# Optimization experiments

Measured on AMD Instinct MI355X. Metric: run time of the kernel, lower is better.

Reference implementation:

```python
import jax, jax.numpy as jnp
import numpy as np

B, C, N, T = 32, 32, 300, 64      # batch, residual/conv channels, nodes, seq_len
DIM, K, SKIP, GD = 40, 20, 64, 2  # node_dim, top-k (subgraph_size), skip_channels, gcn_depth
TANH_A, PROP_A = 3.0, 0.05
KSET = (2, 3, 6, 7)
TOUT = T - (KSET[-1] - 1)          # 58: time length after dilated inception (dilation=1)


def conv2d(x, w, b):
    y = jax.lax.conv_general_dilated(x, w, (1, 1), 'VALID', dimension_numbers=('NCHW', 'OIHW', 'NCHW'))
    return y + b[None, :, None, None]


def setup_inputs() -> dict:
    key = jax.random.key(0)
    ks = iter(jax.random.split(key, 48))
    def nrm(shape, s=1.0):
        return jax.random.normal(next(ks), shape, jnp.float32) * s
    inp = {
        'x': nrm((B, C, N, T)),
        'x_skip': nrm((B, SKIP, N, 1)),
        'idx': jnp.arange(N, dtype=jnp.int32),
        'emb1': nrm((N, DIM), 0.1), 'emb2': nrm((N, DIM), 0.1),
        'lin1_w': nrm((DIM, DIM), 0.15), 'lin1_b': jnp.zeros((DIM,), jnp.float32),
        'lin2_w': nrm((DIM, DIM), 0.15), 'lin2_b': jnp.zeros((DIM,), jnp.float32),
        'skip_w': nrm((SKIP, C, 1, TOUT), 0.05), 'skip_b': jnp.zeros((SKIP,), jnp.float32),
        'mp1_w': nrm((C, (GD + 1) * C, 1, 1), 0.1), 'mp1_b': jnp.zeros((C,), jnp.float32),
        'mp2_w': nrm((C, (GD + 1) * C, 1, 1), 0.1), 'mp2_b': jnp.zeros((C,), jnp.float32),
        'ln_w': jnp.ones((C, N, TOUT), jnp.float32), 'ln_b': jnp.zeros((C, N, TOUT), jnp.float32),
    }
    for k in KSET:
        inp[f'fw{k}'] = nrm((C // 4, C, 1, k), 0.1); inp[f'fb{k}'] = jnp.zeros((C // 4,), jnp.float32)
        inp[f'gw{k}'] = nrm((C // 4, C, 1, k), 0.1); inp[f'gb{k}'] = jnp.zeros((C // 4,), jnp.float32)
    return inp


def _forward(x, x_skip, idx, emb1, emb2, lin1_w, lin1_b, lin2_w, lin2_b,
             fws, gws, skip_w, skip_b, mp1_w, mp1_b, mp2_w, mp2_b, ln_w, ln_b):
    # --- GraphConstructor: learned sparse adjacency via tanh/relu/top-k/scatter ---
    n1 = jnp.tanh(TANH_A * (emb1[idx] @ lin1_w.T + lin1_b))
    n2 = jnp.tanh(TANH_A * (emb2[idx] @ lin2_w.T + lin2_b))
    a = n1 @ n2.T - n2 @ n1.T
    A = jax.nn.relu(jnp.tanh(TANH_A * a))
    _, cols = jax.lax.top_k(A, K)                               # [N, K] per-row top-k indices
    mask = jnp.zeros_like(A).at[jnp.arange(N)[:, None], cols].set(1.0)
    A = A * mask
    # --- DilatedInception filter/gate (Conv2d kernel (1,k), crop to shortest) ---
    Xf = jnp.tanh(jnp.concatenate([conv2d(x, w, b)[..., -TOUT:] for w, b in fws], axis=1))
    Xg = jax.nn.sigmoid(jnp.concatenate([conv2d(x, w, b)[..., -TOUT:] for w, b in gws], axis=1))
    X = Xf * Xg                                                 # dropout is identity (training=False)
    X_skip_out = conv2d(X, skip_w, skip_b) + x_skip             # [B, SKIP, N, 1]
    # --- MixProp graph diffusion over A and A^T ---
    def mixprop(Xin, Adj, w, b):
        Ah = Adj + jnp.eye(N, dtype=Adj.dtype)
        Ah = Ah / Ah.sum(1)[:, None]                            # row-normalize
        H, hops = Xin, [Xin]
        for _ in range(GD):
            H = PROP_A * Xin + (1.0 - PROP_A) * jnp.einsum('bcwt,vw->bcvt', H, Ah)
            hops.append(H)
        return conv2d(jnp.concatenate(hops, axis=1), w, b)      # 1x1 conv: (GD+1)*C -> C
    X = mixprop(X, A, mp1_w, mp1_b) + mixprop(X, A.T, mp2_w, mp2_b)
    X = X + x[..., -TOUT:]
    # --- LayerNorm over (C, N, TOUT) with node-indexed affine ---
    mu = X.mean(axis=(1, 2, 3), keepdims=True)
    var = ((X - mu) ** 2).mean(axis=(1, 2, 3), keepdims=True)
    Xn = (X - mu) * jax.lax.rsqrt(var + 1e-5)
    X = Xn * ln_w[:, idx, :][None] + ln_b[:, idx, :][None]
    return X, X_skip_out


def reference(x, x_skip, idx, emb1, emb2, lin1_w, lin1_b, lin2_w, lin2_b,
              fw2, fb2, fw3, fb3, fw6, fb6, fw7, fb7,
              gw2, gb2, gw3, gb3, gw6, gb6, gw7, gb7,
              skip_w, skip_b, mp1_w, mp1_b, mp2_w, mp2_b, ln_w, ln_b):
    fws = [(fw2, fb2), (fw3, fb3), (fw6, fb6), (fw7, fb7)]
    gws = [(gw2, gb2), (gw3, gb3), (gw6, gb6), (gw7, gb7)]
    return _forward(x, x_skip, idx, emb1, emb2, lin1_w, lin1_b, lin2_w, lin2_b,
                    fws, gws, skip_w, skip_b, mp1_w, mp1_b, mp2_w, mp2_b, ln_w, ln_b)
```

## Files before the change

### kernel.cpp

```cpp
#include <hip/hip_runtime.h>
#include <hip/hip_bf16.h>
#include <math.h>

typedef __hip_bfloat16 bf16;
typedef __attribute__((ext_vector_type(8))) short bf16x8;
typedef __attribute__((ext_vector_type(4))) float f32x4;

#define NB 32
#define NC 32
#define NNODE 300
#define NT 64
#define NDIM 40
#define KTOP 20
#define NSKIP 64
#define NTOUT 58
#define SLAB 17400
#define BSLAB 556800
#define XEL 17817600
#define PSLAB 2048
#define BPSLAB 614400
#define XPEL 19660800

__device__ __forceinline__ float b2f(bf16 v){ return __bfloat162float(v); }
__device__ __forceinline__ bf16 f2b(float v){ return __float2bfloat16(v); }
__device__ __forceinline__ float fsig(float x){ return 1.0f/(1.0f + __expf(-x)); }
__device__ __forceinline__ float ftanh(float x){ return 2.0f*fsig(2.0f*x) - 1.0f; }

__device__ __forceinline__ unsigned short bbits(float v){
  bf16 h = f2b(v); unsigned short s; __builtin_memcpy(&s, &h, 2); return s;
}

__device__ __forceinline__ void fma8(float acc[8], uint4 d, float vv){
  acc[0] = fmaf(vv, __uint_as_float(d.x << 16),          acc[0]);
  acc[1] = fmaf(vv, __uint_as_float(d.x & 0xffff0000u),  acc[1]);
  acc[2] = fmaf(vv, __uint_as_float(d.y << 16),          acc[2]);
  acc[3] = fmaf(vv, __uint_as_float(d.y & 0xffff0000u),  acc[3]);
  acc[4] = fmaf(vv, __uint_as_float(d.z << 16),          acc[4]);
  acc[5] = fmaf(vv, __uint_as_float(d.z & 0xffff0000u),  acc[5]);
  acc[6] = fmaf(vv, __uint_as_float(d.w << 16),          acc[6]);
  acc[7] = fmaf(vv, __uint_as_float(d.w & 0xffff0000u),  acc[7]);
}

__device__ __forceinline__ void unp8(float f[8], uint4 d){
  f[0] = __uint_as_float(d.x << 16); f[1] = __uint_as_float(d.x & 0xffff0000u);
  f[2] = __uint_as_float(d.y << 16); f[3] = __uint_as_float(d.y & 0xffff0000u);
  f[4] = __uint_as_float(d.z << 16); f[5] = __uint_as_float(d.z & 0xffff0000u);
  f[6] = __uint_as_float(d.w << 16); f[7] = __uint_as_float(d.w & 0xffff0000u);
}

__device__ __forceinline__ uint4 pack8(const float f[8]){
  uint4 d;
  d.x = (unsigned)bbits(f[0]) | ((unsigned)bbits(f[1]) << 16);
  d.y = (unsigned)bbits(f[2]) | ((unsigned)bbits(f[3]) << 16);
  d.z = (unsigned)bbits(f[4]) | ((unsigned)bbits(f[5]) << 16);
  d.w = (unsigned)bbits(f[6]) | ((unsigned)bbits(f[7]) << 16);
  return d;
}

__device__ __forceinline__ void bv_swz(int bid, int& b, int& v){
  int xcd = bid & 7, i = bid >> 3;
  int nb = xcd*1200 + i;
  b = nb / NNODE; v = nb - b*NNODE;
}

__global__ void k_nodes(const float* __restrict__ emb1, const float* __restrict__ emb2,
                        const float* __restrict__ l1w, const float* __restrict__ l1b,
                        const float* __restrict__ l2w, const float* __restrict__ l2b,
                        const int* __restrict__ idxp,
                        float* __restrict__ n1, float* __restrict__ n2){
  int i = blockIdx.x; int d = threadIdx.x;
  if (d >= NDIM) return;
  int r = idxp[i];
  float a1 = l1b[d], a2 = l2b[d];
  for (int k=0;k<NDIM;++k){
    a1 = fmaf(emb1[r*NDIM+k], l1w[d*NDIM+k], a1);
    a2 = fmaf(emb2[r*NDIM+k], l2w[d*NDIM+k], a2);
  }
  n1[i*NDIM+d] = tanhf(3.0f*a1);
  n2[i*NDIM+d] = tanhf(3.0f*a2);
}

__global__ void __launch_bounds__(64) k_adjrow(const float* __restrict__ n1,
                                               const float* __restrict__ n2,
                                               float* __restrict__ Am){
  int i = blockIdx.x; int lane = threadIdx.x;
  __shared__ float rowo[NNODE];
  __shared__ float rowv[NNODE];
  __shared__ int   sel[NNODE];
  for (int j=lane;j<NNODE;j+=64){
    float a = 0.f;
    #pragma unroll
    for (int k=0;k<NDIM;++k){
      float a1 = n1[i*NDIM+k], a2 = n2[i*NDIM+k];
      a = fmaf(a1, n2[j*NDIM+k], a);
      a = fmaf(-a2, n1[j*NDIM+k], a);
    }
    float v = tanhf(3.0f*a);
    v = v > 0.f ? v : 0.f;
    rowo[j]=v; rowv[j]=v; sel[j]=0;
  }
  __syncthreads();
  for (int it=0; it<KTOP; ++it){
    float best = -1.f; int bi = 0x7fffffff;
    for (int j=lane;j<NNODE;j+=64){
      float v = rowv[j];
      if (v > best){ best=v; bi=j; }
    }
    #pragma unroll
    for (int off=32; off; off>>=1){
      float ov = __shfl_xor(best, off);
      int   oi = __shfl_xor(bi, off);
      if (ov > best || (ov == best && oi < bi)){ best=ov; bi=oi; }
    }
    if (lane==0){ sel[bi]=1; rowv[bi]=-2.f; }
    __syncthreads();
  }
  for (int j=lane;j<NNODE;j+=64)
    Am[i*NNODE+j] = sel[j] ? rowo[j] : 0.f;
}

__global__ void __launch_bounds__(64) k_csr(const float* __restrict__ Am,
                                            int* __restrict__ aidx, float* __restrict__ aval,
                                            int* __restrict__ acnt){
  int r = blockIdx.x; int lane = threadIdx.x;
  int v = (r < NNODE) ? r : r - NNODE;
  int*   ip = aidx + r*304;
  float* vp = aval + r*304;
  if (lane==0){ ip[0]=v; vp[0]=1.0f; }
  int cnt = 1; float s = 1.0f;
  for (int base=0; base<NNODE; base+=64){
    int j = base + lane; float val = 0.f; bool p = false;
    if (j < NNODE){
      val = (r < NNODE) ? Am[v*NNODE + j] : Am[j*NNODE + v];
      p = val > 0.f;
    }
    unsigned long long m = __ballot(p);
    int pre = __popcll(m & ((1ull << lane) - 1ull));
    if (p){ ip[cnt+pre]=j; vp[cnt+pre]=val; }
    cnt += __popcll(m);
    float vs = p ? val : 0.f;
    #pragma unroll
    for (int off=32; off; off>>=1) vs += __shfl_xor(vs, off);
    s += vs;
  }
  for (int e=lane; e<cnt; e+=64) vp[e] = vp[e] / s;
  if (lane==0) acnt[r]=cnt;
}

__global__ void k_wpack2(const float* __restrict__ fw2,const float* __restrict__ fw3,
                         const float* __restrict__ fw6,const float* __restrict__ fw7,
                         const float* __restrict__ gw2,const float* __restrict__ gw3,
                         const float* __restrict__ gw6,const float* __restrict__ gw7,
                         const float* __restrict__ fb2,const float* __restrict__ fb3,
                         const float* __restrict__ fb6,const float* __restrict__ fb7,
                         const float* __restrict__ gb2,const float* __restrict__ gb3,
                         const float* __restrict__ gb6,const float* __restrict__ gb7,
                         bf16* __restrict__ wfA, float* __restrict__ biasPk){
  int T = blockIdx.x*blockDim.x + threadIdx.x;
  if (T < 14336){
    int j = T & 7;
    int q = T >> 3;
    int l = q & 63; q >>= 6;
    int ks = q % 7, mt = q / 7;
    int m = mt*16 + (l & 15);
    int k = ks*32 + (l >> 4)*8 + j;
    int c = m >> 1, path = m & 1;
    int cls = c >> 3, o = c & 7;
    int ic = k / 7, d = k - ic*7;
    int kk = (cls==0) ? 2 : (cls==1) ? 3 : (cls==2) ? 6 : 7;
    int tp = d - (7 - kk);
    float val = 0.f;
    if (tp >= 0){
      const float* w = (path==0)
        ? (cls==0?fw2:cls==1?fw3:cls==2?fw6:fw7)
        : (cls==0?gw2:cls==1?gw3:cls==2?gw6:gw7);
      val = w[(o*NC + ic)*kk + tp];
    }
    wfA[T] = f2b(val);
  } else if (T < 14336 + 32){
    int c = T - 14336;
    int cls = c >> 3, o = c & 7;
    const float* fb = cls==0?fb2:cls==1?fb3:cls==2?fb6:fb7;
    const float* gb = cls==0?gb2:cls==1?gb3:cls==2?gb6:gb7;
    biasPk[c*2]   = fb[o];
    biasPk[c*2+1] = gb[o];
  }
}

__global__ void k_wprepM(const float* __restrict__ m1w, const float* __restrict__ m2w,
                         const float* __restrict__ m1b, const float* __restrict__ m2b,
                         bf16* __restrict__ pkB, float* __restrict__ biasSum){
  int id = blockIdx.x*blockDim.x + threadIdx.x;
  if (id < 5120){
    int j = id & 7, l = (id >> 3) & 63, q = id >> 9;
    int ks = q % 5, nt = q / 5;
    int k = (l >> 4)*8 + j;
    int c = nt*16 + (l & 15);
    float val;
    if      (ks == 0) val = m1w[c*96 + k] + m2w[c*96 + k];
    else if (ks == 1) val = m1w[c*96 + 32 + k];
    else if (ks == 2) val = m1w[c*96 + 64 + k];
    else if (ks == 3) val = m2w[c*96 + 32 + k];
    else              val = m2w[c*96 + 64 + k];
    pkB[id] = f2b(val);
  } else if (id < 5152){
    int c = id - 5120;
    biasSum[c] = m1b[c] + m2b[c];
  }
}

__global__ void k_wTb(const float* __restrict__ sw, bf16* __restrict__ wTb){
  int id = blockIdx.x*blockDim.x + threadIdx.x;
  if (id >= 131072) return;
  int j = id & 7, l = (id >> 3) & 63, q = id >> 9;
  int ks = q & 63, nt = q >> 6;
  int k = ks*32 + (l >> 4)*8 + j;
  int t = k >> 5, c = k & 31;
  int sc = nt*16 + (l & 15);
  float val = (t < NTOUT) ? sw[sc*1856 + c*NTOUT + t] : 0.f;
  wTb[id] = f2b(val);
}

__global__ void __launch_bounds__(256) k_incepM(const float* __restrict__ x,
    const bf16* __restrict__ wfA, const float* __restrict__ biasPk,
    bf16* __restrict__ Xp){
  __shared__ bf16 xsb[32*72];
  __shared__ uint4 xim2[28*64];
  int b, n; bv_swz(blockIdx.x, b, n);
  int bn = b*NNODE + n;
  int tid = threadIdx.x;
  {
    int c = tid >> 3, t0 = (tid & 7)*8;
    const float* src = x + ((size_t)(b*NC + c)*NNODE + n)*NT + t0;
    float4 v0 = *reinterpret_cast<const float4*>(src);
    float4 v1 = *reinterpret_cast<const float4*>(src + 4);
    float f[8] = {v0.x,v0.y,v0.z,v0.w,v1.x,v1.y,v1.z,v1.w};
    *reinterpret_cast<uint4*>(&xsb[c*72 + t0]) = pack8(f);
    if ((tid & 7) == 7)
      *reinterpret_cast<uint4*>(&xsb[c*72 + 64]) = make_uint4(0,0,0,0);
  }
  __syncthreads();
  #pragma unroll
  for (int i=0;i<7;++i){
    int pr = tid + i*256;
    int kb = pr >> 6, t = pr & 63;
    int k0 = kb*8;
    int ic = k0 / 7, d = k0 - ic*7;
    unsigned sh[8];
    #pragma unroll
    for (int j=0;j<8;++j){
      sh[j] = *reinterpret_cast<const unsigned short*>(&xsb[ic*72 + t + d]);
      ++d; if (d == 7){ d = 0; ++ic; }
    }
    xim2[kb*64 + t] = make_uint4(sh[0]|(sh[1]<<16), sh[2]|(sh[3]<<16),
                                 sh[4]|(sh[5]<<16), sh[6]|(sh[7]<<16));
  }
  __syncthreads();
  int lane = tid & 63;
  int mt = __builtin_amdgcn_readfirstlane(tid >> 6);
  bf16x8 wA[7];
  #pragma unroll
  for (int ks=0; ks<7; ++ks)
    wA[ks] = *reinterpret_cast<const bf16x8*>(wfA + (size_t)((mt*7 + ks)*64 + lane)*8);
  int g = lane >> 4;
  int c0 = mt*8 + 2*g;
  float4 bias2 = *reinterpret_cast<const float4*>(biasPk + c0*2);
  #pragma unroll
  for (int nt=0; nt<4; ++nt){
    int t = (lane & 15) + nt*16;
    f32x4 acc = {0.f, 0.f, 0.f, 0.f};
    #pragma unroll
    for (int ks=0; ks<7; ++ks){
      bf16x8 bfr = __builtin_bit_cast(bf16x8, xim2[(ks*4 + g)*64 + t]);
      acc = __builtin_amdgcn_mfma_f32_16x16x32_bf16(wA[ks], bfr, acc, 0, 0, 0);
    }
    bool act = t < NTOUT;
    float X0 = act ? (ftanh(acc[0] + bias2.x) * fsig(acc[1] + bias2.y)) : 0.f;
    float X1 = act ? (ftanh(acc[2] + bias2.z) * fsig(acc[3] + bias2.w)) : 0.f;
    unsigned pv = (unsigned)bbits(X0) | ((unsigned)bbits(X1) << 16);
    *reinterpret_cast<unsigned*>(Xp + (size_t)bn*PSLAB + t*32 + c0) = pv;
  }
}

__global__ void __launch_bounds__(256) k_skipM(const bf16* __restrict__ Xp, const bf16* __restrict__ wTb,
      const float* __restrict__ skip_b, const float* __restrict__ x_skip, float* __restrict__ out){
  int bn0 = blockIdx.x * 16;
  int tid = threadIdx.x, lane = tid & 63;
  int nt = __builtin_amdgcn_readfirstlane(tid >> 6);
  int g = lane >> 4, col = lane & 15;
  const bf16* aptr = Xp + (size_t)(bn0 + col)*PSLAB + g*8;
  const bf16* bptr = wTb + ((size_t)nt*64*64 + lane)*8;
  f32x4 acc = {0.f, 0.f, 0.f, 0.f};
  #pragma unroll 4
  for (int ks=0; ks<64; ++ks){
    bf16x8 aF = *reinterpret_cast<const bf16x8*>(aptr + ks*32);
    bf16x8 bF = *reinterpret_cast<const bf16x8*>(bptr + (size_t)ks*512);
    acc = __builtin_amdgcn_mfma_f32_16x16x32_bf16(aF, bF, acc, 0, 0, 0);
  }
  int sc = nt*16 + col;
  float sb = skip_b[sc];
  #pragma unroll
  for (int r=0;r<4;++r){
    int bn = bn0 + g*4 + r;
    int b = bn / NNODE, n = bn - b*NNODE;
    size_t so = (size_t)b*NSKIP*NNODE + (size_t)sc*NNODE + n;
    out[(size_t)XEL + so] = acc[r] + sb + x_skip[so];
  }
}

__global__ void __launch_bounds__(256) k_prop(const bf16* __restrict__ Xp,
    bf16* __restrict__ HA0, bf16* __restrict__ HA1,
    const int* __restrict__ aidx, const float* __restrict__ aval, const int* __restrict__ acnt){
  __shared__ int   sidx[304];
  __shared__ float sval[304];
  int bid = blockIdx.x;
  int xcd = bid & 7, i = bid >> 3;
  int side = i & 1, jj = i >> 1;
  int nb = xcd*1200 + jj;
  int b = nb / NNODE, v = nb - b*NNODE;
  int r = (side ? NNODE : 0) + v;
  bf16* HA = side ? HA1 : HA0;
  int cnt = acnt[r];
  for (int e = threadIdx.x; e < cnt; e += 256){
    sidx[e] = aidx[r*304 + e] * PSLAB;
    sval[e] = aval[r*304 + e];
  }
  __syncthreads();
  int t = threadIdx.x >> 2, cb = threadIdx.x & 3;
  int off = t*32 + cb*8;
  const bf16* base = Xp + (size_t)b*BPSLAB + off;
  float acc[8] = {0,0,0,0,0,0,0,0};
  #pragma unroll 4
  for (int j=0;j<cnt;++j){
    uint4 d = *reinterpret_cast<const uint4*>(base + sidx[j]);
    fma8(acc, d, sval[j]);
  }
  size_t own = (size_t)b*BPSLAB + (size_t)v*PSLAB + off;
  uint4 dx = *reinterpret_cast<const uint4*>(Xp + own);
  float xf[8]; unp8(xf, dx);
  float h[8];
  #pragma unroll
  for (int k=0;k<8;++k) h[k] = fmaf(0.95f, acc[k], 0.05f*xf[k]);
  *reinterpret_cast<uint4*>(HA + own) = pack8(h);
}

__global__ void __launch_bounds__(256) k_fuse(const bf16* __restrict__ Xp,
    const bf16* __restrict__ HA0, const bf16* __restrict__ HA1,
    float* __restrict__ out, const float* __restrict__ x,
    const int* __restrict__ aidx, const float* __restrict__ aval, const int* __restrict__ acnt,
    const bf16* __restrict__ pkB, const float* __restrict__ biasSum){
  __shared__ int   sidx0[304];
  __shared__ float sval0[304];
  __shared__ int   sidx1[304];
  __shared__ float sval1[304];
  __shared__ uint4 xs4[320];
  __shared__ uint4 h1a4[320];
  __shared__ uint4 h2a4[320];
  __shared__ uint4 h1b4[320];
  __shared__ uint4 h2b4[320];
  int b, v; bv_swz(blockIdx.x, b, v);
  int r0 = v, r1 = NNODE + v;
  int cnt0 = acnt[r0], cnt1 = acnt[r1];
  for (int e = threadIdx.x; e < cnt0; e += 256){
    sidx0[e] = aidx[r0*304 + e] * PSLAB;
    sval0[e] = aval[r0*304 + e];
  }
  for (int e = threadIdx.x; e < cnt1; e += 256){
    sidx1[e] = aidx[r1*304 + e] * PSLAB;
    sval1[e] = aval[r1*304 + e];
  }
  __syncthreads();
  int tid = threadIdx.x;
  int t = tid >> 2, cb = tid & 3;
  int off = t*32 + cb*8;
  int idx = t*5 + cb;
  size_t bbase = (size_t)b*BPSLAB;
  size_t vbase = bbase + (size_t)v*PSLAB;
  uint4 dx = *reinterpret_cast<const uint4*>(Xp + vbase + off);
  xs4[idx] = dx;
  float xf[8]; unp8(xf, dx);
  h1a4[idx] = *reinterpret_cast<const uint4*>(HA0 + vbase + off);
  h1b4[idx] = *reinterpret_cast<const uint4*>(HA1 + vbase + off);
  {
    const bf16* base = HA0 + bbase + off;
    float acc[8] = {0,0,0,0,0,0,0,0};
    #pragma unroll 4
    for (int j=0;j<cnt0;++j){
      uint4 d = *reinterpret_cast<const uint4*>(base + sidx0[j]);
      fma8(acc, d, sval0[j]);
    }
    float h[8];
    #pragma unroll
    for (int k=0;k<8;++k) h[k] = fmaf(0.95f, acc[k], 0.05f*xf[k]);
    h2a4[idx] = pack8(h);
  }
  {
    const bf16* base = HA1 + bbase + off;
    float acc[8] = {0,0,0,0,0,0,0,0};
    #pragma unroll 4
    for (int j=0;j<cnt1;++j){
      uint4 d = *reinterpret_cast<const uint4*>(base + sidx1[j]);
      fma8(acc, d, sval1[j]);
    }
    float h[8];
    #pragma unroll
    for (int k=0;k<8;++k) h[k] = fmaf(0.95f, acc[k], 0.05f*xf[k]);
    h2b4[idx] = pack8(h);
  }
  __syncthreads();
  int lane = tid & 63;
  int mt = __builtin_amdgcn_readfirstlane(tid >> 6);
  int g = lane >> 4, col = lane & 15;
  int tRow = mt*16 + col;
  int fidx = tRow*5 + g;
  bf16x8 aX  = __builtin_bit_cast(bf16x8, xs4[fidx]);
  bf16x8 a1a = __builtin_bit_cast(bf16x8, h1a4[fidx]);
  bf16x8 a2a = __builtin_bit_cast(bf16x8, h2a4[fidx]);
  bf16x8 a1b = __builtin_bit_cast(bf16x8, h1b4[fidx]);
  bf16x8 a2b = __builtin_bit_cast(bf16x8, h2b4[fidx]);
  int t0 = mt*16 + g*4;
  #pragma unroll
  for (int nt=0; nt<2; ++nt){
    int c_out = nt*16 + col;
    float bv = biasSum[c_out];
    f32x4 acc = {bv, bv, bv, bv};
    bf16x8 w0 = *reinterpret_cast<const bf16x8*>(pkB + (size_t)((nt*5+0)*64 + lane)*8);
    bf16x8 w1 = *reinterpret_cast<const bf16x8*>(pkB + (size_t)((nt*5+1)*64 + lane)*8);
    bf16x8 w2 = *reinterpret_cast<const bf16x8*>(pkB + (size_t)((nt*5+2)*64 + lane)*8);
    bf16x8 w3 = *reinterpret_cast<const bf16x8*>(pkB + (size_t)((nt*5+3)*64 + lane)*8);
    bf16x8 w4 = *reinterpret_cast<const bf16x8*>(pkB + (size_t)((nt*5+4)*64 + lane)*8);
    acc = __builtin_amdgcn_mfma_f32_16x16x32_bf16(aX,  w0, acc, 0, 0, 0);
    acc = __builtin_amdgcn_mfma_f32_16x16x32_bf16(a1a, w1, acc, 0, 0, 0);
    acc = __builtin_amdgcn_mfma_f32_16x16x32_bf16(a2a, w2, acc, 0, 0, 0);
    acc = __builtin_amdgcn_mfma_f32_16x16x32_bf16(a1b, w3, acc, 0, 0, 0);
    acc = __builtin_amdgcn_mfma_f32_16x16x32_bf16(a2b, w4, acc, 0, 0, 0);
    float* po = out + ((size_t)(b*NC + c_out)*NNODE + v)*NTOUT + t0;
    const float* rx = x + ((size_t)(b*NC + c_out)*NNODE + v)*NT + 6 + t0;
    if (t0 <= 54){
      float2 r0v = *reinterpret_cast<const float2*>(rx);
      float2 r1v = *reinterpret_cast<const float2*>(rx + 2);
      *reinterpret_cast<float2*>(po)     = make_float2(acc[0] + r0v.x, acc[1] + r0v.y);
      *reinterpret_cast<float2*>(po + 2) = make_float2(acc[2] + r1v.x, acc[3] + r1v.y);
    } else if (t0 == 56){
      float2 r0v = *reinterpret_cast<const float2*>(rx);
      *reinterpret_cast<float2*>(po)     = make_float2(acc[0] + r0v.x, acc[1] + r0v.y);
    }
  }
}

__global__ void __launch_bounds__(256) k_lnstat(const float* __restrict__ out, double* __restrict__ part){
  int blk = blockIdx.x; int b = blk >> 3, seg = blk & 7;
  const float* p = out + (size_t)b*BSLAB;
  int start = seg*69600, end = start + 69600;
  double s = 0.0, s2 = 0.0;
  for (int i = start + threadIdx.x; i < end; i += 256){
    double v = (double)p[i]; s += v; s2 += v*v;
  }
  #pragma unroll
  for (int off=32; off; off>>=1){ s += __shfl_down(s, off); s2 += __shfl_down(s2, off); }
  __shared__ double ls[4], ls2[4];
  int lane = threadIdx.x & 63, w = threadIdx.x >> 6;
  if (lane==0){ ls[w]=s; ls2[w]=s2; }
  __syncthreads();
  if (threadIdx.x==0){
    double a=0.0, a2=0.0;
    for (int i=0;i<4;++i){ a+=ls[i]; a2+=ls2[i]; }
    part[blk*2]=a; part[blk*2+1]=a2;
  }
}

__global__ void k_lnfin(const double* __restrict__ part, float* __restrict__ stats){
  int b = threadIdx.x; if (b >= 32) return;
  double s=0.0, s2=0.0;
  for (int seg=0; seg<8; ++seg){ s += part[(b*8+seg)*2]; s2 += part[(b*8+seg)*2+1]; }
  double n = (double)BSLAB;
  double mean = s/n;
  double var = s2/n - mean*mean;
  stats[b*2]   = (float)mean;
  stats[b*2+1] = (float)(1.0/sqrt(var + 1e-5));
}

__global__ void __launch_bounds__(256) k_lnapply(float* __restrict__ out, const float* __restrict__ stats,
        const float* __restrict__ lnw, const float* __restrict__ lnb, const int* __restrict__ idxp){
  int o = blockIdx.x*256 + threadIdx.x;
  int t = o % NTOUT; int v = (o / NTOUT) % NNODE; int c = (o / SLAB) % NC; int b = o / BSLAB;
  float mean = stats[b*2], rstd = stats[b*2+1];
  int vn = idxp[v];
  float wv = lnw[((size_t)c*NNODE + vn)*NTOUT + t];
  float bv = lnb[((size_t)c*NNODE + vn)*NTOUT + t];
  float vx = out[o];
  out[o] = (vx - mean)*rstd*wv + bv;
}

extern "C" void kernel_launch(void* const* d_in, const int* in_sizes, int n_in,
                              void* d_out, int out_size, void* d_ws, size_t ws_size,
                              hipStream_t stream) {
  (void)in_sizes; (void)n_in; (void)out_size; (void)ws_size;
  const float* x     = (const float*)d_in[0];
  const float* xskip = (const float*)d_in[1];
  const int*   idxp  = (const int*)d_in[2];
  const float* emb1  = (const float*)d_in[3];
  const float* emb2  = (const float*)d_in[4];
  const float* l1w   = (const float*)d_in[5];
  const float* l1b   = (const float*)d_in[6];
  const float* l2w   = (const float*)d_in[7];
  const float* l2b   = (const float*)d_in[8];
  const float* skw   = (const float*)d_in[9];
  const float* skb   = (const float*)d_in[10];
  const float* m1w   = (const float*)d_in[11];
  const float* m1b   = (const float*)d_in[12];
  const float* m2w   = (const float*)d_in[13];
  const float* m2b   = (const float*)d_in[14];
  const float* lnw   = (const float*)d_in[15];
  const float* lnb   = (const float*)d_in[16];
  const float* fw2=(const float*)d_in[17]; const float* fb2=(const float*)d_in[18];
  const float* gw2=(const float*)d_in[19]; const float* gb2=(const float*)d_in[20];
  const float* fw3=(const float*)d_in[21]; const float* fb3=(const float*)d_in[22];
  const float* gw3=(const float*)d_in[23]; const float* gb3=(const float*)d_in[24];
  const float* fw6=(const float*)d_in[25]; const float* fb6=(const float*)d_in[26];
  const float* gw6=(const float*)d_in[27]; const float* gb6=(const float*)d_in[28];
  const float* fw7=(const float*)d_in[29]; const float* fb7=(const float*)d_in[30];
  const float* gw7=(const float*)d_in[31]; const float* gb7=(const float*)d_in[32];
  float* out = (float*)d_out;

  char* wsbase = (char*)d_ws;
  size_t cur = 0;
  auto alloc = [&](size_t bytes)->char*{
    char* p = wsbase + cur;
    cur = (cur + bytes + 255) & ~(size_t)255;
    return p;
  };
  bf16*  Xp   = (bf16*) alloc((size_t)XPEL*2);
  bf16*  HA0  = (bf16*) alloc((size_t)XPEL*2);
  bf16*  HA1  = (bf16*) alloc((size_t)XPEL*2);
  float* n1   = (float*)alloc(12000*4);
  float* n2   = (float*)alloc(12000*4);
  float* Am   = (float*)alloc(90000*4);
  int*   aidx = (int*)  alloc(600*304*4);
  float* aval = (float*)alloc(600*304*4);
  int*   acnt = (int*)  alloc(600*4);
  bf16*  wTb  = (bf16*) alloc(131072*2);
  bf16*  wfA  = (bf16*) alloc(14336*2);
  float* biasPk = (float*)alloc(64*4);
  bf16*  pkB  = (bf16*) alloc(5120*2);
  float* biasSum = (float*)alloc(32*4);
  double* part = (double*)alloc(256*2*8);
  float* stats = (float*)alloc(64*4);

  k_nodes <<<NNODE, 64, 0, stream>>>(emb1, emb2, l1w, l1b, l2w, l2b, idxp, n1, n2);
  k_adjrow<<<NNODE, 64, 0, stream>>>(n1, n2, Am);
  k_csr   <<<2*NNODE, 64, 0, stream>>>(Am, aidx, aval, acnt);

  k_wpack2<<<57, 256, 0, stream>>>(fw2,fw3,fw6,fw7, gw2,gw3,gw6,gw7,
                                   fb2,fb3,fb6,fb7, gb2,gb3,gb6,gb7, wfA, biasPk);
  k_wprepM<<<21, 256, 0, stream>>>(m1w, m2w, m1b, m2b, pkB, biasSum);
  k_wTb   <<<512, 256, 0, stream>>>(skw, wTb);

  k_incepM<<<NB*NNODE, 256, 0, stream>>>(x, wfA, biasPk, Xp);

  k_skipM<<<(NB*NNODE)/16, 256, 0, stream>>>(Xp, wTb, skb, xskip, out);

  k_prop<<<2*NB*NNODE, 256, 0, stream>>>(Xp, HA0, HA1, aidx, aval, acnt);

  k_fuse<<<NB*NNODE, 256, 0, stream>>>(Xp, HA0, HA1, out, x, aidx, aval, acnt, pkB, biasSum);

  k_lnstat<<<256, 256, 0, stream>>>(out, part);
  k_lnfin<<<1, 32, 0, stream>>>(part, stats);
  k_lnapply<<<XEL/256, 256, 0, stream>>>(out, stats, lnw, lnb, idxp);
}
```

Measured before the change: 448.7 us.

## Fuse LayerNorm statistics into k_fuse and split propagation sides across 512 threads

k_fuse now runs 512 threads per block, so the two second-hop propagation sides (A and A^T) are computed in parallel by separate halves instead of one after the other. Each wave also computes a single MFMA output tile, with A operands read straight from global memory rather than staged in LDS. The per-batch sum and sum-of-squares for LayerNorm are reduced inside k_fuse and accumulated with double atomics, which removes the separate k_lnstat pass over the whole output. In exchange the partial sums are kept in float per block, the atomics add contention on 32 addresses, and a memset is added to clear the accumulators.

```diff
diff --git a/kernel.cpp b/kernel.cpp
--- a/kernel.cpp
+++ b/kernel.cpp
@@ -344,86 +344,65 @@
   *reinterpret_cast<uint4*>(HA + own) = pack8(h);
 }
 
-__global__ void __launch_bounds__(256) k_fuse(const bf16* __restrict__ Xp,
+__global__ void __launch_bounds__(512) k_fuse(const bf16* __restrict__ Xp,
     const bf16* __restrict__ HA0, const bf16* __restrict__ HA1,
     float* __restrict__ out, const float* __restrict__ x,
     const int* __restrict__ aidx, const float* __restrict__ aval, const int* __restrict__ acnt,
-    const bf16* __restrict__ pkB, const float* __restrict__ biasSum){
-  __shared__ int   sidx0[304];
-  __shared__ float sval0[304];
-  __shared__ int   sidx1[304];
-  __shared__ float sval1[304];
-  __shared__ uint4 xs4[320];
-  __shared__ uint4 h1a4[320];
-  __shared__ uint4 h2a4[320];
-  __shared__ uint4 h1b4[320];
-  __shared__ uint4 h2b4[320];
+    const bf16* __restrict__ pkB, const float* __restrict__ biasSum,
+    double* __restrict__ part2){
+  __shared__ int   sidx[2][304];
+  __shared__ float sval[2][304];
+  __shared__ uint4 h2s[2][320];
+  __shared__ float redS[8], redS2[8];
   int b, v; bv_swz(blockIdx.x, b, v);
-  int r0 = v, r1 = NNODE + v;
-  int cnt0 = acnt[r0], cnt1 = acnt[r1];
-  for (int e = threadIdx.x; e < cnt0; e += 256){
-    sidx0[e] = aidx[r0*304 + e] * PSLAB;
-    sval0[e] = aval[r0*304 + e];
-  }
-  for (int e = threadIdx.x; e < cnt1; e += 256){
-    sidx1[e] = aidx[r1*304 + e] * PSLAB;
-    sval1[e] = aval[r1*304 + e];
-  }
-  __syncthreads();
   int tid = threadIdx.x;
-  int t = tid >> 2, cb = tid & 3;
-  int off = t*32 + cb*8;
-  int idx = t*5 + cb;
+  int side = tid >> 8;
+  int st = tid & 255;
+  int r = side*NNODE + v;
+  int cnt = acnt[r];
+  for (int e = st; e < cnt; e += 256){
+    sidx[side][e] = aidx[r*304 + e] * PSLAB;
+    sval[side][e] = aval[r*304 + e];
+  }
+  __syncthreads();
   size_t bbase = (size_t)b*BPSLAB;
   size_t vbase = bbase + (size_t)v*PSLAB;
-  uint4 dx = *reinterpret_cast<const uint4*>(Xp + vbase + off);
-  xs4[idx] = dx;
-  float xf[8]; unp8(xf, dx);
-  h1a4[idx] = *reinterpret_cast<const uint4*>(HA0 + vbase + off);
-  h1b4[idx] = *reinterpret_cast<const uint4*>(HA1 + vbase + off);
   {
-    const bf16* base = HA0 + bbase + off;
+    int t = st >> 2, cb = st & 3;
+    int off = t*32 + cb*8;
+    const bf16* HH = side ? HA1 : HA0;
+    const bf16* base = HH + bbase + off;
+    const int*   si = sidx[side];
+    const float* sv = sval[side];
     float acc[8] = {0,0,0,0,0,0,0,0};
     #pragma unroll 4
-    for (int j=0;j<cnt0;++j){
-      uint4 d = *reinterpret_cast<const uint4*>(base + sidx0[j]);
-      fma8(acc, d, sval0[j]);
-    }
+    for (int j=0;j<cnt;++j){
+      uint4 d = *reinterpret_cast<const uint4*>(base + si[j]);
+      fma8(acc, d, sv[j]);
+    }
+    uint4 dx = *reinterpret_cast<const uint4*>(Xp + vbase + off);
+    float xf[8]; unp8(xf, dx);
     float h[8];
     #pragma unroll
     for (int k=0;k<8;++k) h[k] = fmaf(0.95f, acc[k], 0.05f*xf[k]);
-    h2a4[idx] = pack8(h);
-  }
-  {
-    const bf16* base = HA1 + bbase + off;
-    float acc[8] = {0,0,0,0,0,0,0,0};
-    #pragma unroll 4
-    for (int j=0;j<cnt1;++j){
-      uint4 d = *reinterpret_cast<const uint4*>(base + sidx1[j]);
-      fma8(acc, d, sval1[j]);
-    }
-    float h[8];
-    #pragma unroll
-    for (int k=0;k<8;++k) h[k] = fmaf(0.95f, acc[k], 0.05f*xf[k]);
-    h2b4[idx] = pack8(h);
+    h2s[side][t*5 + cb] = pack8(h);
   }
   __syncthreads();
   int lane = tid & 63;
-  int mt = __builtin_amdgcn_readfirstlane(tid >> 6);
+  int wave = __builtin_amdgcn_readfirstlane(tid >> 6);
+  int mt = wave & 3, nt = wave >> 2;
   int g = lane >> 4, col = lane & 15;
   int tRow = mt*16 + col;
-  int fidx = tRow*5 + g;
-  bf16x8 aX  = __builtin_bit_cast(bf16x8, xs4[fidx]);
-  bf16x8 a1a = __builtin_bit_cast(bf16x8, h1a4[fidx]);
-  bf16x8 a2a = __builtin_bit_cast(bf16x8, h2a4[fidx]);
-  bf16x8 a1b = __builtin_bit_cast(bf16x8, h1b4[fidx]);
-  bf16x8 a2b = __builtin_bit_cast(bf16x8, h2b4[fidx]);
-  int t0 = mt*16 + g*4;
-  #pragma unroll
-  for (int nt=0; nt<2; ++nt){
-    int c_out = nt*16 + col;
-    float bv = biasSum[c_out];
-    f32x4 acc = {bv, bv, bv, bv};
+  const bf16* slab = Xp + vbase + tRow*32 + g*8;
+  bf16x8 aX  = *reinterpret_cast<const bf16x8*>(slab);
+  bf16x8 a1a = *reinterpret_cast<const bf16x8*>(HA0 + vbase + tRow*32 + g*8);
+  bf16x8 a1b = *reinterpret_cast<const bf16x8*>(HA1 + vbase + tRow*32 + g*8);
+  bf16x8 a2a = __builtin_bit_cast(bf16x8, h2s[0][tRow*5 + g]);
+  bf16x8 a2b = __builtin_bit_cast(bf16x8, h2s[1][tRow*5 + g]);
+  int c_out = nt*16 + col;
+  float bv = biasSum[c_out];
+  f32x4 acc = {bv, bv, bv, bv};
+  {
     bf16x8 w0 = *reinterpret_cast<const bf16x8*>(pkB + (size_t)((nt*5+0)*64 + lane)*8);
     bf16x8 w1 = *reinterpret_cast<const bf16x8*>(pkB + (size_t)((nt*5+1)*64 + lane)*8);
     bf16x8 w2 = *reinterpret_cast<const bf16x8*>(pkB + (size_t)((nt*5+2)*64 + lane)*8);
@@ -434,45 +413,43 @@
     acc = __builtin_amdgcn_mfma_f32_16x16x32_bf16(a2a, w2, acc, 0, 0, 0);
     acc = __builtin_amdgcn_mfma_f32_16x16x32_bf16(a1b, w3, acc, 0, 0, 0);
     acc = __builtin_amdgcn_mfma_f32_16x16x32_bf16(a2b, w4, acc, 0, 0, 0);
-    float* po = out + ((size_t)(b*NC + c_out)*NNODE + v)*NTOUT + t0;
-    const float* rx = x + ((size_t)(b*NC + c_out)*NNODE + v)*NT + 6 + t0;
-    if (t0 <= 54){
-      float2 r0v = *reinterpret_cast<const float2*>(rx);
-      float2 r1v = *reinterpret_cast<const float2*>(rx + 2);
-      *reinterpret_cast<float2*>(po)     = make_float2(acc[0] + r0v.x, acc[1] + r0v.y);
-      *reinterpret_cast<float2*>(po + 2) = make_float2(acc[2] + r1v.x, acc[3] + r1v.y);
-    } else if (t0 == 56){
-      float2 r0v = *reinterpret_cast<const float2*>(rx);
-      *reinterpret_cast<float2*>(po)     = make_float2(acc[0] + r0v.x, acc[1] + r0v.y);
-    }
-  }
-}
-
-__global__ void __launch_bounds__(256) k_lnstat(const float* __restrict__ out, double* __restrict__ part){
-  int blk = blockIdx.x; int b = blk >> 3, seg = blk & 7;
-  const float* p = out + (size_t)b*BSLAB;
-  int start = seg*69600, end = start + 69600;
-  double s = 0.0, s2 = 0.0;
-  for (int i = start + threadIdx.x; i < end; i += 256){
-    double v = (double)p[i]; s += v; s2 += v*v;
+  }
+  int t0 = mt*16 + g*4;
+  float s = 0.f, s2 = 0.f;
+  float* po = out + ((size_t)(b*NC + c_out)*NNODE + v)*NTOUT + t0;
+  const float* rx = x + ((size_t)(b*NC + c_out)*NNODE + v)*NT + 6 + t0;
+  if (t0 <= 54){
+    float2 r0v = *reinterpret_cast<const float2*>(rx);
+    float2 r1v = *reinterpret_cast<const float2*>(rx + 2);
+    float o0 = acc[0] + r0v.x, o1 = acc[1] + r0v.y;
+    float o2 = acc[2] + r1v.x, o3 = acc[3] + r1v.y;
+    *reinterpret_cast<float2*>(po)     = make_float2(o0, o1);
+    *reinterpret_cast<float2*>(po + 2) = make_float2(o2, o3);
+    s  = o0 + o1 + o2 + o3;
+    s2 = o0*o0 + o1*o1 + o2*o2 + o3*o3;
+  } else if (t0 == 56){
+    float2 r0v = *reinterpret_cast<const float2*>(rx);
+    float o0 = acc[0] + r0v.x, o1 = acc[1] + r0v.y;
+    *reinterpret_cast<float2*>(po) = make_float2(o0, o1);
+    s  = o0 + o1;
+    s2 = o0*o0 + o1*o1;
   }
   #pragma unroll
-  for (int off=32; off; off>>=1){ s += __shfl_down(s, off); s2 += __shfl_down(s2, off); }
-  __shared__ double ls[4], ls2[4];
-  int lane = threadIdx.x & 63, w = threadIdx.x >> 6;
-  if (lane==0){ ls[w]=s; ls2[w]=s2; }
-  __syncthreads();
-  if (threadIdx.x==0){
-    double a=0.0, a2=0.0;
-    for (int i=0;i<4;++i){ a+=ls[i]; a2+=ls2[i]; }
-    part[blk*2]=a; part[blk*2+1]=a2;
-  }
-}
-
-__global__ void k_lnfin(const double* __restrict__ part, float* __restrict__ stats){
+  for (int o=32; o; o>>=1){ s += __shfl_down(s, o); s2 += __shfl_down(s2, o); }
+  if (lane == 0){ redS[wave] = s; redS2[wave] = s2; }
+  __syncthreads();
+  if (tid == 0){
+    float as = 0.f, as2 = 0.f;
+    #pragma unroll
+    for (int w=0; w<8; ++w){ as += redS[w]; as2 += redS2[w]; }
+    atomicAdd(&part2[b*2],   (double)as);
+    atomicAdd(&part2[b*2+1], (double)as2);
+  }
+}
+
+__global__ void k_lnfin(const double* __restrict__ part2, float* __restrict__ stats){
   int b = threadIdx.x; if (b >= 32) return;
-  double s=0.0, s2=0.0;
-  for (int seg=0; seg<8; ++seg){ s += part[(b*8+seg)*2]; s2 += part[(b*8+seg)*2+1]; }
+  double s = part2[b*2], s2 = part2[b*2+1];
   double n = (double)BSLAB;
   double mean = s/n;
   double var = s2/n - mean*mean;
@@ -544,8 +521,10 @@
   float* biasPk = (float*)alloc(64*4);
   bf16*  pkB  = (bf16*) alloc(5120*2);
   float* biasSum = (float*)alloc(32*4);
-  double* part = (double*)alloc(256*2*8);
+  double* part2 = (double*)alloc(64*8);
   float* stats = (float*)alloc(64*4);
+
+  hipMemsetAsync(part2, 0, 64*sizeof(double), stream);
 
   k_nodes <<<NNODE, 64, 0, stream>>>(emb1, emb2, l1w, l1b, l2w, l2b, idxp, n1, n2);
   k_adjrow<<<NNODE, 64, 0, stream>>>(n1, n2, Am);
@@ -562,9 +541,8 @@
 
   k_prop<<<2*NB*NNODE, 256, 0, stream>>>(Xp, HA0, HA1, aidx, aval, acnt);
 
-  k_fuse<<<NB*NNODE, 256, 0, stream>>>(Xp, HA0, HA1, out, x, aidx, aval, acnt, pkB, biasSum);
-
-  k_lnstat<<<256, 256, 0, stream>>>(out, part);
-  k_lnfin<<<1, 32, 0, stream>>>(part, stats);
+  k_fuse<<<NB*NNODE, 512, 0, stream>>>(Xp, HA0, HA1, out, x, aidx, aval, acnt, pkB, biasSum, part2);
+
+  k_lnfin<<<1, 32, 0, stream>>>(part2, stats);
   k_lnapply<<<XEL/256, 256, 0, stream>>>(out, stats, lnw, lnb, idxp);
 }
```

New measurement: 367.8 us. -18.0%, faster.
